# Optimization experiments

Hardware: AMD Instinct MI355X
Metric: run time of the kernel (lower is better)

The kernel has to match this reference:

```python
import jax, jax.numpy as jnp
import numpy as np

N_HEAD = 16
HEAD_DIM = 64
EPS_RMS = 1e-6


def _rope(x, cos, sin):
    # x: [B, T, H, D]; cos/sin: [T, D//2] broadcast to [1, T, 1, D//2]
    d2 = x.shape[-1] // 2
    x1, x2 = x[..., :d2], x[..., d2:]
    c = cos[None, :, None, :]
    s = sin[None, :, None, :]
    return jnp.concatenate([x1 * c + x2 * s, -x1 * s + x2 * c], axis=-1)


def _rms_norm(x):
    return x * jax.lax.rsqrt(jnp.mean(x * x, axis=-1, keepdims=True) + EPS_RMS)


def setup_inputs() -> dict:
    key = jax.random.key(0)
    ks = jax.random.split(key, 7)
    B, T, C = 1, 4096, 1024
    x = jax.random.normal(ks[0], (B, T, C), dtype=jnp.float32)
    # realistic rotary angles
    d2 = HEAD_DIM // 2
    inv_freq = 1.0 / (10000.0 ** (np.arange(0, d2, dtype=np.float32) / d2))
    ang = np.arange(T, dtype=np.float32)[:, None] * inv_freq[None, :]
    cos = jnp.asarray(np.cos(ang), dtype=jnp.float32)
    sin = jnp.asarray(np.sin(ang), dtype=jnp.float32)
    scale = 0.02
    wq = jax.random.normal(ks[1], (C, C), dtype=jnp.float32) * scale
    wk = jax.random.normal(ks[2], (C, C), dtype=jnp.float32) * scale
    wv = jax.random.normal(ks[3], (C, C), dtype=jnp.float32) * scale
    wproj = jax.random.normal(ks[4], (C, C), dtype=jnp.float32) * scale
    return {"x": x, "cos": cos, "sin": sin, "wq": wq, "wk": wk, "wv": wv, "wproj": wproj}


def reference(x, cos, sin, wq, wk, wv, wproj):
    B, T, C = x.shape
    H, D = N_HEAD, HEAD_DIM
    # QKV projections (torch Linear: x @ W.T)
    q = (x @ wq.T).reshape(B, T, H, D)
    k = (x @ wk.T).reshape(B, T, H, D)
    v = (x @ wv.T).reshape(B, T, H, D)
    # RoPE then QK RMS-norm
    q = _rms_norm(_rope(q, cos, sin))
    k = _rms_norm(_rope(k, cos, sin))
    # [B, H, T, D]
    q = q.transpose(0, 2, 1, 3)
    k = k.transpose(0, 2, 1, 3)
    v = v.transpose(0, 2, 1, 3)
    scores = jnp.einsum('bhqd,bhkd->bhqk', q, k) * (1.0 / D ** 0.5)
    # causal mask (kv_cache is None, Tq == Tk == T)
    mask = jnp.tril(jnp.ones((T, T), dtype=bool))
    scores = jnp.where(mask[None, None, :, :], scores, -jnp.inf)
    attn = jax.nn.sigmoid(scores)  # sigmoid(-inf) == 0
    y = jnp.einsum('bhqk,bhkd->bhqd', attn, v)
    y = y / (T ** 0.5 + 1e-6)
    y = y.transpose(0, 2, 1, 3).reshape(B, T, C)
    return y @ wproj.T
```

## Files before the change

### kernel.cpp

```cpp
#include <hip/hip_runtime.h>

typedef __attribute__((ext_vector_type(8))) short bf16x8;
typedef __attribute__((ext_vector_type(4))) float f32x4;
typedef __attribute__((ext_vector_type(16))) float f32x16;

__device__ inline f32x4 mfma16(bf16x8 a, bf16x8 b, f32x4 c) {
    return __builtin_amdgcn_mfma_f32_16x16x32_bf16(a, b, c, 0, 0, 0);
}
__device__ inline f32x16 mfma32(bf16x8 a, bf16x8 b, f32x16 c) {
    return __builtin_amdgcn_mfma_f32_32x32x16_bf16(a, b, c, 0, 0, 0);
}

__device__ inline short f2bf(float f) {
    unsigned u = __builtin_bit_cast(unsigned, f);
    unsigned r = (u + 0x7fffu + ((u >> 16) & 1u)) >> 16;
    return (short)r;
}
__device__ inline float bf2f(short h) {
    unsigned u = ((unsigned)(unsigned short)h) << 16;
    return __builtin_bit_cast(float, u);
}

__device__ inline unsigned cvt_pk_bf16(float lo, float hi) {
    unsigned r;
    asm("v_cvt_pk_bf16_f32 %0, %1, %2" : "=v"(r) : "v"(lo), "v"(hi));
    return r;
}
__device__ inline void plane_swap(unsigned& a, unsigned& b) {
    asm("v_permlane32_swap_b32 %0, %1" : "+v"(a), "+v"(b));
}
__device__ inline float exp2_hw(float x) {
    float r;
    asm("v_exp_f32 %0, %1" : "=v"(r) : "v"(x));
    return r;
}

#define GAS(p) (const __attribute__((address_space(1))) void*)(p)
#define LAS(p) (__attribute__((address_space(3))) void*)(p)

#define T_SEQ 4096
#define C_DIM 1024
#define N_HEAD 16
#define HEAD_DIM 64
#define QSCALE (-0.18033688011112042f)

__global__ __launch_bounds__(256) void cast5(
    const float* __restrict__ s0, const float* __restrict__ s1,
    const float* __restrict__ s2, const float* __restrict__ s3,
    const float* __restrict__ s4,
    short* __restrict__ d0, short* __restrict__ d1, short* __restrict__ d2,
    short* __restrict__ d3, short* __restrict__ d4,
    int n0, int n1, int n2, int n3, int n4)
{
    int z = blockIdx.y;
    const float* s; short* d; int n;
    switch (z) {
        case 0: s = s0; d = d0; n = n0; break;
        case 1: s = s1; d = d1; n = n1; break;
        case 2: s = s2; d = d2; n = n2; break;
        case 3: s = s3; d = d3; n = n3; break;
        default: s = s4; d = d4; n = n4; break;
    }
    int i = (blockIdx.x * 256 + threadIdx.x) * 4;
    if (i >= n) return;
    float4 v = *(const float4*)&s[i];
    short4 o;
    o.x = f2bf(v.x); o.y = f2bf(v.y); o.z = f2bf(v.z); o.w = f2bf(v.w);
    *(short4*)&d[i] = o;
}

template<int OBF>
__global__ __launch_bounds__(256) void gemm3(
    const short* __restrict__ A,
    const short* __restrict__ B0, const short* __restrict__ B1,
    const short* __restrict__ B2,
    void* C0, void* C1, void* C2,
    int M, int N, int K)
{
    const short* B = (blockIdx.z == 0) ? B0 : ((blockIdx.z == 1) ? B1 : B2);
    void*        C = (blockIdx.z == 0) ? C0 : ((blockIdx.z == 1) ? C1 : C2);

    __shared__ alignas(16) short sA[128 * 32];
    __shared__ alignas(16) short sB[128 * 32];

    int tid  = threadIdx.x;
    int wave = tid >> 6, lane = tid & 63;
    int lhi  = lane >> 4, llo = lane & 15;
    int wr   = wave >> 1, wc = wave & 1;
    int row0 = blockIdx.x * 128, col0 = blockIdx.y * 128;

    int srow = lane >> 2;
    int scol = (lane & 3) * 8;

    f32x4 acc[4][4];
#pragma unroll
    for (int m = 0; m < 4; m++)
#pragma unroll
        for (int n = 0; n < 4; n++)
            acc[m][n] = (f32x4){0.f, 0.f, 0.f, 0.f};

    for (int k0 = 0; k0 < K; k0 += 32) {
        __syncthreads();
#pragma unroll
        for (int s2 = 0; s2 < 2; s2++) {
            int rbase = wave * 32 + s2 * 16;
            __builtin_amdgcn_global_load_lds(
                GAS(&A[(size_t)(row0 + rbase + srow) * K + k0 + scol]),
                LAS(&sA[rbase * 32]), 16, 0, 0);
            __builtin_amdgcn_global_load_lds(
                GAS(&B[(size_t)(col0 + rbase + srow) * K + k0 + scol]),
                LAS(&sB[rbase * 32]), 16, 0, 0);
        }
        __syncthreads();

        bf16x8 af[4], bfv[4];
#pragma unroll
        for (int m = 0; m < 4; m++)
            af[m] = *(const bf16x8*)&sA[(wr * 64 + m * 16 + llo) * 32 + lhi * 8];
#pragma unroll
        for (int n = 0; n < 4; n++)
            bfv[n] = *(const bf16x8*)&sB[(wc * 64 + n * 16 + llo) * 32 + lhi * 8];
#pragma unroll
        for (int m = 0; m < 4; m++)
#pragma unroll
            for (int n = 0; n < 4; n++)
                acc[m][n] = mfma16(af[m], bfv[n], acc[m][n]);
    }

#pragma unroll
    for (int m = 0; m < 4; m++)
#pragma unroll
        for (int n = 0; n < 4; n++)
#pragma unroll
            for (int r = 0; r < 4; r++) {
                int row = row0 + wr * 64 + m * 16 + lhi * 4 + r;
                int col = col0 + wc * 64 + n * 16 + llo;
                float v = acc[m][n][r];
                if (OBF) ((short*)C)[(size_t)row * N + col] = f2bf(v);
                else     ((float*)C)[(size_t)row * N + col] = v;
            }
}

__global__ __launch_bounds__(256) void rope2(
    const short* __restrict__ Qb, const short* __restrict__ Kb,
    const float* __restrict__ cosT, const float* __restrict__ sinT,
    short* __restrict__ qnb, short* __restrict__ knb)
{
    int z = blockIdx.y;
    const short* src = z ? Kb : Qb;
    short* dst = z ? knb : qnb;
    float osc = z ? 1.0f : QSCALE;

    int rowg = blockIdx.x * 32 + (threadIdx.x >> 3);
    int t = rowg >> 4, h = rowg & 15;
    int j = threadIdx.x & 7;

    bf16x8 v8 = *(const bf16x8*)&src[(size_t)t * C_DIM + h * HEAD_DIM + j * 8];
    float f[8], o[8];
#pragma unroll
    for (int i = 0; i < 8; i++) f[i] = bf2f(v8[i]);
#pragma unroll
    for (int i = 0; i < 8; i++) o[i] = __shfl_xor(f[i], 4);

    const float* cp = &cosT[t * 32 + (j & 3) * 8];
    const float* sp = &sinT[t * 32 + (j & 3) * 8];
    float4 c0 = *(const float4*)&cp[0], c1 = *(const float4*)&cp[4];
    float4 s0 = *(const float4*)&sp[0], s1 = *(const float4*)&sp[4];
    float cc[8] = {c0.x, c0.y, c0.z, c0.w, c1.x, c1.y, c1.z, c1.w};
    float ss[8] = {s0.x, s0.y, s0.z, s0.w, s1.x, s1.y, s1.z, s1.w};

    float r[8];
    if (j < 4) {
#pragma unroll
        for (int i = 0; i < 8; i++) r[i] = f[i] * cc[i] + o[i] * ss[i];
    } else {
#pragma unroll
        for (int i = 0; i < 8; i++) r[i] = f[i] * cc[i] - o[i] * ss[i];
    }

    float sq = 0.f;
#pragma unroll
    for (int i = 0; i < 8; i++) sq += r[i] * r[i];
#pragma unroll
    for (int off = 1; off <= 4; off <<= 1) sq += __shfl_xor(sq, off);
    float inv = rsqrtf(sq * (1.0f / 64.0f) + 1e-6f) * osc;

    bf16x8 out;
#pragma unroll
    for (int i = 0; i < 8; i++) out[i] = f2bf(r[i] * inv);
    *(bf16x8*)&dst[((size_t)h * T_SEQ + t) * HEAD_DIM + j * 8] = out;
}

__global__ __launch_bounds__(256) void vtrans(
    const short* __restrict__ Vb, short* __restrict__ vt)
{
    __shared__ short sT[64 * 65];
    int h = blockIdx.y, tb = blockIdx.x;
    int tid = threadIdx.x;
    const float inv64 = 1.0f / (64.0f + 1e-6f);
#pragma unroll
    for (int i = 0; i < 16; i++) {
        int linear = i * 256 + tid;
        int r = linear >> 6, c = linear & 63;
        float v = bf2f(Vb[(size_t)(tb * 64 + r) * C_DIM + h * HEAD_DIM + c]) * inv64;
        sT[c * 65 + r] = f2bf(v);
    }
    __syncthreads();
#pragma unroll
    for (int i = 0; i < 16; i++) {
        int linear = i * 256 + tid;
        int dd = linear >> 6, tt = linear & 63;
        vt[((size_t)(h * HEAD_DIM + dd)) * T_SEQ + tb * 64 + tt] = sT[dd * 65 + tt];
    }
}


#define STAGE6(s_, bf_) do {                                                     \
    int kb_ = (s_) * 64;                                                         \
    int r_  = lane >> 3;                                                         \
    int ss_ = (lane & 7) ^ r_;                                                   \
    __builtin_amdgcn_global_load_lds(                                            \
        GAS(Kh + (size_t)(kb_ + wv * 16 + r_) * HEAD_DIM + ss_ * 8),             \
        LAS(Smem + (bf_) * 8192 + (wv * 16) * 128), 16, 0, 0);                   \
    __builtin_amdgcn_global_load_lds(                                            \
        GAS(Kh + (size_t)(kb_ + wv * 16 + 8 + r_) * HEAD_DIM + ss_ * 8),         \
        LAS(Smem + (bf_) * 8192 + (wv * 16 + 8) * 128), 16, 0, 0);               \
    __builtin_amdgcn_global_load_lds(                                            \
        GAS(Vh + (size_t)(wv * 16 + r_) * T_SEQ + kb_ + ss_ * 8),                \
        LAS(Smem + 16384 + (bf_) * 8192 + (wv * 16) * 128), 16, 0, 0);           \
    __builtin_amdgcn_global_load_lds(                                            \
        GAS(Vh + (size_t)(wv * 16 + 8 + r_) * T_SEQ + kb_ + ss_ * 8),            \
        LAS(Smem + 16384 + (bf_) * 8192 + (wv * 16 + 8) * 128), 16, 0, 0);       \
} while (0)

__global__ __launch_bounds__(256, 4) void attn6(
    const short* __restrict__ qn, const short* __restrict__ kn,
    const short* __restrict__ vt, short* __restrict__ yb)
{
    __shared__ alignas(16) char Smem[32768];

    int id = blockIdx.x;
    int h  = id & 15;
    int g  = id >> 4;
    int t  = (g < 16) ? (63 - g) : (g < 32) ? (g - 16)
           : (g < 48) ? (79 - g) : (g - 32);
    int ns = t + 1;

    int tid = threadIdx.x, wv = tid >> 6, lane = tid & 63;
    int lo = lane & 31, hi = lane >> 5;
    int band = wv & 1, tm = wv >> 1;

    const short* Qh = qn + (size_t)h * T_SEQ * HEAD_DIM;
    const short* Kh = kn + (size_t)h * T_SEQ * HEAD_DIM;
    const short* Vh = vt + (size_t)h * HEAD_DIM * T_SEQ;

    int q0 = t * 64;
    int qrow  = q0 + band * 32 + lo;
    int qmaxw = q0 + band * 32 + 31;

    const short* Qr = &Qh[(size_t)qrow * HEAD_DIM + hi * 8];
    bf16x8 qf0 = *(const bf16x8*)&Qr[0];
    bf16x8 qf1 = *(const bf16x8*)&Qr[16];
    bf16x8 qf2 = *(const bf16x8*)&Qr[32];
    bf16x8 qf3 = *(const bf16x8*)&Qr[48];

    f32x16 zed;
#pragma unroll
    for (int r = 0; r < 16; r++) zed[r] = 0.f;

    f32x16 yac0, yac1;
#pragma unroll
    for (int r = 0; r < 16; r++) { yac0[r] = 0.f; yac1[r] = 0.f; }

    unsigned sw   = (unsigned)((lo & 7) << 4);
    unsigned krow = (unsigned)((tm * 32 + lo) * 128);
    unsigned ko0 = krow + ((0u * 32 + hi * 16) ^ sw);
    unsigned ko1 = krow + ((1u * 32 + hi * 16) ^ sw);
    unsigned ko2 = krow + ((2u * 32 + hi * 16) ^ sw);
    unsigned ko3 = krow + ((3u * 32 + hi * 16) ^ sw);
    unsigned vrow0 = (unsigned)(lo * 128)        + 16384u;
    unsigned vrow1 = (unsigned)((32 + lo) * 128) + 16384u;
    unsigned vo00 = vrow0 + (((unsigned)(tm * 64 + 0 * 32 + hi * 16)) ^ sw);
    unsigned vo01 = vrow0 + (((unsigned)(tm * 64 + 1 * 32 + hi * 16)) ^ sw);
    unsigned vo10 = vrow1 + (((unsigned)(tm * 64 + 0 * 32 + hi * 16)) ^ sw);
    unsigned vo11 = vrow1 + (((unsigned)(tm * 64 + 1 * 32 + hi * 16)) ^ sw);

    STAGE6(0, 0);
    int buf = 0;
    for (int s = 0; s < ns; s++) {
        if (s + 1 < ns) {
            STAGE6(s + 1, buf ^ 1);
            asm volatile("s_waitcnt vmcnt(4)" ::: "memory");
        } else {
            asm volatile("s_waitcnt vmcnt(0)" ::: "memory");
        }
        __builtin_amdgcn_s_barrier();

        int kb0 = s * 64 + tm * 32;
        if (kb0 <= qmaxw) {
            const char* B_ = Smem + (buf << 13);
            bf16x8 kf0 = *(const bf16x8*)(B_ + ko0);
            bf16x8 kf1 = *(const bf16x8*)(B_ + ko1);
            bf16x8 kf2 = *(const bf16x8*)(B_ + ko2);
            bf16x8 kf3 = *(const bf16x8*)(B_ + ko3);
            bf16x8 vf00 = *(const bf16x8*)(B_ + vo00);
            bf16x8 vf01 = *(const bf16x8*)(B_ + vo01);
            bf16x8 vf10 = *(const bf16x8*)(B_ + vo10);
            bf16x8 vf11 = *(const bf16x8*)(B_ + vo11);

            f32x16 sv;
            __builtin_amdgcn_s_setprio(1);
            sv = mfma32(kf0, qf0, zed);
            sv = mfma32(kf1, qf1, sv);
            sv = mfma32(kf2, qf2, sv);
            sv = mfma32(kf3, qf3, sv);
            __builtin_amdgcn_s_setprio(0);

            if (kb0 + 31 > q0 + band * 32) {
#pragma unroll
                for (int r = 0; r < 16; r++) {
                    int kvg = kb0 + (r & 3) + 8 * (r >> 2) + 4 * hi;
                    float pv = __builtin_amdgcn_rcpf(1.f + exp2_hw(sv[r]));
                    sv[r] = (kvg <= qrow) ? pv : 0.f;
                }
            } else {
#pragma unroll
                for (int r = 0; r < 16; r++)
                    sv[r] = __builtin_amdgcn_rcpf(1.f + exp2_hw(sv[r]));
            }

#pragma unroll
            for (int k2 = 0; k2 < 2; k2++) {
                unsigned wA = cvt_pk_bf16(sv[8 * k2 + 0], sv[8 * k2 + 1]);
                unsigned wC = cvt_pk_bf16(sv[8 * k2 + 2], sv[8 * k2 + 3]);
                unsigned wB = cvt_pk_bf16(sv[8 * k2 + 4], sv[8 * k2 + 5]);
                unsigned wD = cvt_pk_bf16(sv[8 * k2 + 6], sv[8 * k2 + 7]);
                plane_swap(wA, wB);
                plane_swap(wC, wD);
                union { unsigned u[4]; bf16x8 v; } pw;
                pw.u[0] = wA; pw.u[1] = wC; pw.u[2] = wB; pw.u[3] = wD;
                __builtin_amdgcn_s_setprio(1);
                yac0 = mfma32(pw.v, k2 ? vf01 : vf00, yac0);
                yac1 = mfma32(pw.v, k2 ? vf11 : vf10, yac1);
                __builtin_amdgcn_s_setprio(0);
            }
        }
        asm volatile("" ::: "memory");
        __builtin_amdgcn_s_barrier();
        buf ^= 1;
    }

    __syncthreads();
    float* Yred = (float*)Smem;
    if (tm == 1) {
#pragma unroll
        for (int d = 0; d < 2; d++)
#pragma unroll
            for (int r = 0; r < 16; r++) {
                int crow = (r & 3) + 8 * (r >> 2) + 4 * hi;
                Yred[(band * 32 + crow) * 64 + d * 32 + lo] = d ? yac1[r] : yac0[r];
            }
    }
    __syncthreads();
    if (tm == 0) {
#pragma unroll
        for (int d = 0; d < 2; d++)
#pragma unroll
            for (int r = 0; r < 16; r++) {
                int crow = (r & 3) + 8 * (r >> 2) + 4 * hi;
                float v = (d ? yac1[r] : yac0[r]) + Yred[(band * 32 + crow) * 64 + d * 32 + lo];
                yb[(size_t)(q0 + band * 32 + crow) * C_DIM + h * HEAD_DIM + d * 32 + lo] = f2bf(v);
            }
    }
}

extern "C" void kernel_launch(void* const* d_in, const int* in_sizes, int n_in,
                              void* d_out, int out_size, void* d_ws, size_t ws_size,
                              hipStream_t stream)
{
    const float* x    = (const float*)d_in[0];
    const float* cosT = (const float*)d_in[1];
    const float* sinT = (const float*)d_in[2];
    const float* wq   = (const float*)d_in[3];
    const float* wk   = (const float*)d_in[4];
    const float* wv   = (const float*)d_in[5];
    const float* wp   = (const float*)d_in[6];

    char* ws = (char*)d_ws;
    const size_t MB = 1024 * 1024;
    short* xb  = (short*)(ws + 0);
    short* wqb = (short*)(ws + 8  * MB);
    short* wkb = (short*)(ws + 10 * MB);
    short* wvb = (short*)(ws + 12 * MB);
    short* wpb = (short*)(ws + 14 * MB);
    short* Qb  = (short*)(ws + 16 * MB);
    short* Kb  = (short*)(ws + 24 * MB);
    short* Vb  = (short*)(ws + 32 * MB);
    short* qnb = (short*)(ws + 40 * MB);
    short* knb = (short*)(ws + 48 * MB);
    short* vtb = (short*)(ws + 56 * MB);
    short* yb  = (short*)(ws + 64 * MB);

    cast5<<<dim3(4096, 5, 1), 256, 0, stream>>>(
        x, wq, wk, wv, wp, xb, wqb, wkb, wvb, wpb,
        T_SEQ * C_DIM, C_DIM * C_DIM, C_DIM * C_DIM, C_DIM * C_DIM, C_DIM * C_DIM);

    gemm3<1><<<dim3(32, 8, 3), 256, 0, stream>>>(
        xb, wqb, wkb, wvb, (void*)Qb, (void*)Kb, (void*)Vb, T_SEQ, C_DIM, C_DIM);

    rope2<<<dim3(2048, 2, 1), 256, 0, stream>>>(Qb, Kb, cosT, sinT, qnb, knb);

    vtrans<<<dim3(64, 16, 1), 256, 0, stream>>>(Vb, vtb);

    attn6<<<1024, 256, 0, stream>>>(qnb, knb, vtb, yb);

    gemm3<0><<<dim3(32, 8, 1), 256, 0, stream>>>(
        yb, wpb, wpb, wpb, d_out, d_out, d_out, T_SEQ, C_DIM, C_DIM);
}
```

Measured before the change: 142.3 us.

## Fuse RoPE/RMS-norm into QKV GEMM epilogue and split attention KV blocks in two

The QKV GEMM epilogue now applies RoPE and RMS-norm in registers and writes head-major Q/K/V directly, which removes the separate rope2 kernel and its round-trip of the intermediate Q/K tensors. The attention kernel is split across two blocks per (query tile, head), with even and odd KV blocks going to different blocks. Each block writes a bf16 partial, and a new comb kernel sums the two partials. This doubles the grid to improve load balance and occupancy, and occupancy is raised to 5 blocks per CU. In exchange it adds an extra kernel, extra partial-buffer traffic, and a second bf16 rounding of the output.

New measurement: 251.2 us. 1.77x slower.

```diff
diff --git a/kernel.cpp b/kernel.cpp
--- a/kernel.cpp
+++ b/kernel.cpp
@@ -69,17 +69,110 @@
     *(short4*)&d[i] = o;
 }
 
-template<int OBF>
-__global__ __launch_bounds__(256) void gemm3(
+__global__ __launch_bounds__(256) void gemm_qkv(
     const short* __restrict__ A,
     const short* __restrict__ B0, const short* __restrict__ B1,
     const short* __restrict__ B2,
-    void* C0, void* C1, void* C2,
-    int M, int N, int K)
-{
-    const short* B = (blockIdx.z == 0) ? B0 : ((blockIdx.z == 1) ? B1 : B2);
-    void*        C = (blockIdx.z == 0) ? C0 : ((blockIdx.z == 1) ? C1 : C2);
-
+    short* __restrict__ qnb, short* __restrict__ knb, short* __restrict__ vnb,
+    const float* __restrict__ cosT, const float* __restrict__ sinT)
+{
+    int z = blockIdx.z;
+    const short* B = (z == 0) ? B0 : ((z == 1) ? B1 : B2);
+    short* dst     = (z == 0) ? qnb : ((z == 1) ? knb : vnb);
+
+    __shared__ alignas(16) short sA[128 * 32];
+    __shared__ alignas(16) short sB[128 * 32];
+
+    int tid  = threadIdx.x;
+    int wave = tid >> 6, lane = tid & 63;
+    int lhi  = lane >> 4, llo = lane & 15;
+    int wr   = wave >> 1, wc = wave & 1;
+    int row0 = blockIdx.x * 128, col0 = blockIdx.y * 128;
+
+    int srow = lane >> 2;
+    int scol = (lane & 3) * 8;
+
+    f32x4 acc[4][4];
+#pragma unroll
+    for (int m = 0; m < 4; m++)
+#pragma unroll
+        for (int n = 0; n < 4; n++)
+            acc[m][n] = (f32x4){0.f, 0.f, 0.f, 0.f};
+
+    for (int k0 = 0; k0 < C_DIM; k0 += 32) {
+        __syncthreads();
+#pragma unroll
+        for (int s2 = 0; s2 < 2; s2++) {
+            int rbase = wave * 32 + s2 * 16;
+            __builtin_amdgcn_global_load_lds(
+                GAS(&A[(size_t)(row0 + rbase + srow) * C_DIM + k0 + scol]),
+                LAS(&sA[rbase * 32]), 16, 0, 0);
+            __builtin_amdgcn_global_load_lds(
+                GAS(&B[(size_t)(col0 + rbase + srow) * C_DIM + k0 + scol]),
+                LAS(&sB[rbase * 32]), 16, 0, 0);
+        }
+        __syncthreads();
+
+        bf16x8 af[4], bfv[4];
+#pragma unroll
+        for (int m = 0; m < 4; m++)
+            af[m] = *(const bf16x8*)&sA[(wr * 64 + m * 16 + llo) * 32 + lhi * 8];
+#pragma unroll
+        for (int n = 0; n < 4; n++)
+            bfv[n] = *(const bf16x8*)&sB[(wc * 64 + n * 16 + llo) * 32 + lhi * 8];
+#pragma unroll
+        for (int m = 0; m < 4; m++)
+#pragma unroll
+            for (int n = 0; n < 4; n++)
+                acc[m][n] = mfma16(af[m], bfv[n], acc[m][n]);
+    }
+
+    int hH = blockIdx.y * 2 + wc;
+    if (z < 2) {
+        float osc = z ? 1.0f : QSCALE;
+#pragma unroll
+        for (int m = 0; m < 4; m++)
+#pragma unroll
+            for (int r = 0; r < 4; r++) {
+                int row = row0 + wr * 64 + m * 16 + lhi * 4 + r;
+                float c0 = cosT[row * 32 + llo],      c1 = cosT[row * 32 + 16 + llo];
+                float s0 = sinT[row * 32 + llo],      s1 = sinT[row * 32 + 16 + llo];
+                float e0 = acc[m][0][r], e1 = acc[m][1][r];
+                float e2 = acc[m][2][r], e3 = acc[m][3][r];
+                float r0 = e0 * c0 + e2 * s0;
+                float r1 = e1 * c1 + e3 * s1;
+                float r2 = e2 * c0 - e0 * s0;
+                float r3 = e3 * c1 - e1 * s1;
+                float sq = r0 * r0 + r1 * r1 + r2 * r2 + r3 * r3;
+                sq += __shfl_xor(sq, 1);
+                sq += __shfl_xor(sq, 2);
+                sq += __shfl_xor(sq, 4);
+                sq += __shfl_xor(sq, 8);
+                float inv = rsqrtf(sq * (1.0f / 64.0f) + 1e-6f) * osc;
+                size_t base = ((size_t)hH * T_SEQ + row) * HEAD_DIM + llo;
+                dst[base +  0] = f2bf(r0 * inv);
+                dst[base + 16] = f2bf(r1 * inv);
+                dst[base + 32] = f2bf(r2 * inv);
+                dst[base + 48] = f2bf(r3 * inv);
+            }
+    } else {
+#pragma unroll
+        for (int m = 0; m < 4; m++)
+#pragma unroll
+            for (int r = 0; r < 4; r++) {
+                int row = row0 + wr * 64 + m * 16 + lhi * 4 + r;
+                size_t base = ((size_t)hH * T_SEQ + row) * HEAD_DIM + llo;
+#pragma unroll
+                for (int n = 0; n < 4; n++)
+                    dst[base + n * 16] = f2bf(acc[m][n][r]);
+            }
+    }
+}
+
+__global__ __launch_bounds__(256) void gemm_proj(
+    const short* __restrict__ A, const short* __restrict__ B,
+    float* __restrict__ C, int M, int N, int K)
+{
     __shared__ alignas(16) short sA[128 * 32];
     __shared__ alignas(16) short sB[128 * 32];
 
@@ -135,64 +228,12 @@
             for (int r = 0; r < 4; r++) {
                 int row = row0 + wr * 64 + m * 16 + lhi * 4 + r;
                 int col = col0 + wc * 64 + n * 16 + llo;
-                float v = acc[m][n][r];
-                if (OBF) ((short*)C)[(size_t)row * N + col] = f2bf(v);
-                else     ((float*)C)[(size_t)row * N + col] = v;
-            }
-}
-
-__global__ __launch_bounds__(256) void rope2(
-    const short* __restrict__ Qb, const short* __restrict__ Kb,
-    const float* __restrict__ cosT, const float* __restrict__ sinT,
-    short* __restrict__ qnb, short* __restrict__ knb)
-{
-    int z = blockIdx.y;
-    const short* src = z ? Kb : Qb;
-    short* dst = z ? knb : qnb;
-    float osc = z ? 1.0f : QSCALE;
-
-    int rowg = blockIdx.x * 32 + (threadIdx.x >> 3);
-    int t = rowg >> 4, h = rowg & 15;
-    int j = threadIdx.x & 7;
-
-    bf16x8 v8 = *(const bf16x8*)&src[(size_t)t * C_DIM + h * HEAD_DIM + j * 8];
-    float f[8], o[8];
-#pragma unroll
-    for (int i = 0; i < 8; i++) f[i] = bf2f(v8[i]);
-#pragma unroll
-    for (int i = 0; i < 8; i++) o[i] = __shfl_xor(f[i], 4);
-
-    const float* cp = &cosT[t * 32 + (j & 3) * 8];
-    const float* sp = &sinT[t * 32 + (j & 3) * 8];
-    float4 c0 = *(const float4*)&cp[0], c1 = *(const float4*)&cp[4];
-    float4 s0 = *(const float4*)&sp[0], s1 = *(const float4*)&sp[4];
-    float cc[8] = {c0.x, c0.y, c0.z, c0.w, c1.x, c1.y, c1.z, c1.w};
-    float ss[8] = {s0.x, s0.y, s0.z, s0.w, s1.x, s1.y, s1.z, s1.w};
-
-    float r[8];
-    if (j < 4) {
-#pragma unroll
-        for (int i = 0; i < 8; i++) r[i] = f[i] * cc[i] + o[i] * ss[i];
-    } else {
-#pragma unroll
-        for (int i = 0; i < 8; i++) r[i] = f[i] * cc[i] - o[i] * ss[i];
-    }
-
-    float sq = 0.f;
-#pragma unroll
-    for (int i = 0; i < 8; i++) sq += r[i] * r[i];
-#pragma unroll
-    for (int off = 1; off <= 4; off <<= 1) sq += __shfl_xor(sq, off);
-    float inv = rsqrtf(sq * (1.0f / 64.0f) + 1e-6f) * osc;
-
-    bf16x8 out;
-#pragma unroll
-    for (int i = 0; i < 8; i++) out[i] = f2bf(r[i] * inv);
-    *(bf16x8*)&dst[((size_t)h * T_SEQ + t) * HEAD_DIM + j * 8] = out;
+                C[(size_t)row * N + col] = acc[m][n][r];
+            }
 }
 
 __global__ __launch_bounds__(256) void vtrans(
-    const short* __restrict__ Vb, short* __restrict__ vt)
+    const short* __restrict__ vnb, short* __restrict__ vt)
 {
     __shared__ short sT[64 * 65];
     int h = blockIdx.y, tb = blockIdx.x;
@@ -202,7 +243,7 @@
     for (int i = 0; i < 16; i++) {
         int linear = i * 256 + tid;
         int r = linear >> 6, c = linear & 63;
-        float v = bf2f(Vb[(size_t)(tb * 64 + r) * C_DIM + h * HEAD_DIM + c]) * inv64;
+        float v = bf2f(vnb[((size_t)h * T_SEQ + tb * 64 + r) * HEAD_DIM + c]) * inv64;
         sT[c * 65 + r] = f2bf(v);
     }
     __syncthreads();
@@ -233,18 +274,22 @@
         LAS(Smem + 16384 + (bf_) * 8192 + (wv * 16 + 8) * 128), 16, 0, 0);       \
 } while (0)
 
-__global__ __launch_bounds__(256, 4) void attn6(
+__global__ __launch_bounds__(256, 5) void attn7(
     const short* __restrict__ qn, const short* __restrict__ kn,
-    const short* __restrict__ vt, short* __restrict__ yb)
+    const short* __restrict__ vt, short* __restrict__ part0,
+    short* __restrict__ part1)
 {
     __shared__ alignas(16) char Smem[32768];
 
-    int id = blockIdx.x;
-    int h  = id & 15;
-    int g  = id >> 4;
-    int t  = (g < 16) ? (63 - g) : (g < 32) ? (g - 16)
-           : (g < 48) ? (79 - g) : (g - 32);
-    int ns = t + 1;
+    int j = blockIdx.x;
+    int p = j & 1;
+    int h = (j >> 1) & 15;
+    int u = j >> 5;
+    int kk = u >> 3, bb = u & 7;
+    int base = (kk >> 1) * 8 + bb;
+    int t = (kk & 1) ? base : (63 - base);
+
+    short* part = p ? part1 : part0;
 
     int tid = threadIdx.x, wv = tid >> 6, lane = tid & 63;
     int lo = lane & 31, hi = lane >> 5;
@@ -256,6 +301,7 @@
 
     int q0 = t * 64;
     int qrow  = q0 + band * 32 + lo;
+    int qminw = q0 + band * 32;
     int qmaxw = q0 + band * 32 + 31;
 
     const short* Qr = &Qh[(size_t)qrow * HEAD_DIM + hi * 8];
@@ -285,69 +331,71 @@
     unsigned vo10 = vrow1 + (((unsigned)(tm * 64 + 0 * 32 + hi * 16)) ^ sw);
     unsigned vo11 = vrow1 + (((unsigned)(tm * 64 + 1 * 32 + hi * 16)) ^ sw);
 
-    STAGE6(0, 0);
-    int buf = 0;
-    for (int s = 0; s < ns; s++) {
-        if (s + 1 < ns) {
-            STAGE6(s + 1, buf ^ 1);
-            asm volatile("s_waitcnt vmcnt(4)" ::: "memory");
-        } else {
-            asm volatile("s_waitcnt vmcnt(0)" ::: "memory");
+    if (p <= t) {
+        STAGE6(p, 0);
+        int buf = 0;
+        for (int s = p; s <= t; s += 2) {
+            if (s + 2 <= t) {
+                STAGE6(s + 2, buf ^ 1);
+                asm volatile("s_waitcnt vmcnt(4)" ::: "memory");
+            } else {
+                asm volatile("s_waitcnt vmcnt(0)" ::: "memory");
+            }
+            __builtin_amdgcn_s_barrier();
+
+            int kb0 = s * 64 + tm * 32;
+            if (kb0 <= qmaxw) {
+                const char* B_ = Smem + (buf << 13);
+                bf16x8 kf0 = *(const bf16x8*)(B_ + ko0);
+                bf16x8 kf1 = *(const bf16x8*)(B_ + ko1);
+                bf16x8 kf2 = *(const bf16x8*)(B_ + ko2);
+                bf16x8 kf3 = *(const bf16x8*)(B_ + ko3);
+                bf16x8 vf00 = *(const bf16x8*)(B_ + vo00);
+                bf16x8 vf01 = *(const bf16x8*)(B_ + vo01);
+                bf16x8 vf10 = *(const bf16x8*)(B_ + vo10);
+                bf16x8 vf11 = *(const bf16x8*)(B_ + vo11);
+
+                f32x16 sv;
+                __builtin_amdgcn_s_setprio(1);
+                sv = mfma32(kf0, qf0, zed);
+                sv = mfma32(kf1, qf1, sv);
+                sv = mfma32(kf2, qf2, sv);
+                sv = mfma32(kf3, qf3, sv);
+                __builtin_amdgcn_s_setprio(0);
+
+                if (kb0 + 31 > qminw) {
+#pragma unroll
+                    for (int r = 0; r < 16; r++) {
+                        int kvg = kb0 + (r & 3) + 8 * (r >> 2) + 4 * hi;
+                        float pv = __builtin_amdgcn_rcpf(1.f + exp2_hw(sv[r]));
+                        sv[r] = (kvg <= qrow) ? pv : 0.f;
+                    }
+                } else {
+#pragma unroll
+                    for (int r = 0; r < 16; r++)
+                        sv[r] = __builtin_amdgcn_rcpf(1.f + exp2_hw(sv[r]));
+                }
+
+#pragma unroll
+                for (int k2 = 0; k2 < 2; k2++) {
+                    unsigned wA = cvt_pk_bf16(sv[8 * k2 + 0], sv[8 * k2 + 1]);
+                    unsigned wC = cvt_pk_bf16(sv[8 * k2 + 2], sv[8 * k2 + 3]);
+                    unsigned wB = cvt_pk_bf16(sv[8 * k2 + 4], sv[8 * k2 + 5]);
+                    unsigned wD = cvt_pk_bf16(sv[8 * k2 + 6], sv[8 * k2 + 7]);
+                    plane_swap(wA, wB);
+                    plane_swap(wC, wD);
+                    union { unsigned u[4]; bf16x8 v; } pw;
+                    pw.u[0] = wA; pw.u[1] = wC; pw.u[2] = wB; pw.u[3] = wD;
+                    __builtin_amdgcn_s_setprio(1);
+                    yac0 = mfma32(pw.v, k2 ? vf01 : vf00, yac0);
+                    yac1 = mfma32(pw.v, k2 ? vf11 : vf10, yac1);
+                    __builtin_amdgcn_s_setprio(0);
+                }
+            }
+            asm volatile("" ::: "memory");
+            __builtin_amdgcn_s_barrier();
+            buf ^= 1;
         }
-        __builtin_amdgcn_s_barrier();
-
-        int kb0 = s * 64 + tm * 32;
-        if (kb0 <= qmaxw) {
-            const char* B_ = Smem + (buf << 13);
-            bf16x8 kf0 = *(const bf16x8*)(B_ + ko0);
-            bf16x8 kf1 = *(const bf16x8*)(B_ + ko1);
-            bf16x8 kf2 = *(const bf16x8*)(B_ + ko2);
-            bf16x8 kf3 = *(const bf16x8*)(B_ + ko3);
-            bf16x8 vf00 = *(const bf16x8*)(B_ + vo00);
-            bf16x8 vf01 = *(const bf16x8*)(B_ + vo01);
-            bf16x8 vf10 = *(const bf16x8*)(B_ + vo10);
-            bf16x8 vf11 = *(const bf16x8*)(B_ + vo11);
-
-            f32x16 sv;
-            __builtin_amdgcn_s_setprio(1);
-            sv = mfma32(kf0, qf0, zed);
-            sv = mfma32(kf1, qf1, sv);
-            sv = mfma32(kf2, qf2, sv);
-            sv = mfma32(kf3, qf3, sv);
-            __builtin_amdgcn_s_setprio(0);
-
-            if (kb0 + 31 > q0 + band * 32) {
-#pragma unroll
-                for (int r = 0; r < 16; r++) {
-                    int kvg = kb0 + (r & 3) + 8 * (r >> 2) + 4 * hi;
-                    float pv = __builtin_amdgcn_rcpf(1.f + exp2_hw(sv[r]));
-                    sv[r] = (kvg <= qrow) ? pv : 0.f;
-                }
-            } else {
-#pragma unroll
-                for (int r = 0; r < 16; r++)
-                    sv[r] = __builtin_amdgcn_rcpf(1.f + exp2_hw(sv[r]));
-            }
-
-#pragma unroll
-            for (int k2 = 0; k2 < 2; k2++) {
-                unsigned wA = cvt_pk_bf16(sv[8 * k2 + 0], sv[8 * k2 + 1]);
-                unsigned wC = cvt_pk_bf16(sv[8 * k2 + 2], sv[8 * k2 + 3]);
-                unsigned wB = cvt_pk_bf16(sv[8 * k2 + 4], sv[8 * k2 + 5]);
-                unsigned wD = cvt_pk_bf16(sv[8 * k2 + 6], sv[8 * k2 + 7]);
-                plane_swap(wA, wB);
-                plane_swap(wC, wD);
-                union { unsigned u[4]; bf16x8 v; } pw;
-                pw.u[0] = wA; pw.u[1] = wC; pw.u[2] = wB; pw.u[3] = wD;
-                __builtin_amdgcn_s_setprio(1);
-                yac0 = mfma32(pw.v, k2 ? vf01 : vf00, yac0);
-                yac1 = mfma32(pw.v, k2 ? vf11 : vf10, yac1);
-                __builtin_amdgcn_s_setprio(0);
-            }
-        }
-        asm volatile("" ::: "memory");
-        __builtin_amdgcn_s_barrier();
-        buf ^= 1;
     }
 
     __syncthreads();
@@ -369,9 +417,22 @@
             for (int r = 0; r < 16; r++) {
                 int crow = (r & 3) + 8 * (r >> 2) + 4 * hi;
                 float v = (d ? yac1[r] : yac0[r]) + Yred[(band * 32 + crow) * 64 + d * 32 + lo];
-                yb[(size_t)(q0 + band * 32 + crow) * C_DIM + h * HEAD_DIM + d * 32 + lo] = f2bf(v);
-            }
-    }
+                part[(size_t)(q0 + band * 32 + crow) * C_DIM + h * HEAD_DIM + d * 32 + lo] = f2bf(v);
+            }
+    }
+}
+
+__global__ __launch_bounds__(256) void comb(
+    const short* __restrict__ p0, const short* __restrict__ p1,
+    short* __restrict__ yb)
+{
+    int i = (blockIdx.x * 256 + threadIdx.x) * 8;
+    bf16x8 a = *(const bf16x8*)&p0[i];
+    bf16x8 b = *(const bf16x8*)&p1[i];
+    bf16x8 o;
+#pragma unroll
+    for (int j = 0; j < 8; j++) o[j] = f2bf(bf2f(a[j]) + bf2f(b[j]));
+    *(bf16x8*)&yb[i] = o;
 }
 
 extern "C" void kernel_launch(void* const* d_in, const int* in_sizes, int n_in,
@@ -388,32 +449,32 @@
 
     char* ws = (char*)d_ws;
     const size_t MB = 1024 * 1024;
-    short* xb  = (short*)(ws + 0);
-    short* wqb = (short*)(ws + 8  * MB);
-    short* wkb = (short*)(ws + 10 * MB);
-    short* wvb = (short*)(ws + 12 * MB);
-    short* wpb = (short*)(ws + 14 * MB);
-    short* Qb  = (short*)(ws + 16 * MB);
-    short* Kb  = (short*)(ws + 24 * MB);
-    short* Vb  = (short*)(ws + 32 * MB);
-    short* qnb = (short*)(ws + 40 * MB);
-    short* knb = (short*)(ws + 48 * MB);
-    short* vtb = (short*)(ws + 56 * MB);
-    short* yb  = (short*)(ws + 64 * MB);
+    short* xb    = (short*)(ws + 0);
+    short* wqb   = (short*)(ws + 8  * MB);
+    short* wkb   = (short*)(ws + 10 * MB);
+    short* wvb   = (short*)(ws + 12 * MB);
+    short* wpb   = (short*)(ws + 14 * MB);
+    short* qnb   = (short*)(ws + 16 * MB);
+    short* knb   = (short*)(ws + 24 * MB);
+    short* vnb   = (short*)(ws + 32 * MB);
+    short* vtb   = (short*)(ws + 40 * MB);
+    short* yb    = (short*)(ws + 48 * MB);
+    short* part0 = (short*)(ws + 56 * MB);
+    short* part1 = (short*)(ws + 64 * MB);
 
     cast5<<<dim3(4096, 5, 1), 256, 0, stream>>>(
         x, wq, wk, wv, wp, xb, wqb, wkb, wvb, wpb,
         T_SEQ * C_DIM, C_DIM * C_DIM, C_DIM * C_DIM, C_DIM * C_DIM, C_DIM * C_DIM);
 
-    gemm3<1><<<dim3(32, 8, 3), 256, 0, stream>>>(
-        xb, wqb, wkb, wvb, (void*)Qb, (void*)Kb, (void*)Vb, T_SEQ, C_DIM, C_DIM);
-
-    rope2<<<dim3(2048, 2, 1), 256, 0, stream>>>(Qb, Kb, cosT, sinT, qnb, knb);
-
-    vtrans<<<dim3(64, 16, 1), 256, 0, stream>>>(Vb, vtb);
-
-    attn6<<<1024, 256, 0, stream>>>(qnb, knb, vtb, yb);
-
-    gemm3<0><<<dim3(32, 8, 1), 256, 0, stream>>>(
-        yb, wpb, wpb, wpb, d_out, d_out, d_out, T_SEQ, C_DIM, C_DIM);
-}
+    gemm_qkv<<<dim3(32, 8, 3), 256, 0, stream>>>(
+        xb, wqb, wkb, wvb, qnb, knb, vnb, cosT, sinT);
+
+    vtrans<<<dim3(64, 16, 1), 256, 0, stream>>>(vnb, vtb);
+
+    attn7<<<2048, 256, 0, stream>>>(qnb, knb, vtb, part0, part1);
+
+    comb<<<2048, 256, 0, stream>>>(part0, part1, yb);
+
+    gemm_proj<<<dim3(32, 8, 1), 256, 0, stream>>>(
+        yb, wpb, (float*)d_out, T_SEQ, C_DIM, C_DIM);
+}
```
